# Kernel tuning notes

Hardware: AMD Instinct MI355X
Metric: run time of the kernel (lower is better)

Reference implementation:

```python
import jax, jax.numpy as jnp
import numpy as np

TOPK = 60            # candidates kept by top-k
THRESHOLD = 0.15     # score threshold (post-sigmoid)
NMS_THRESHOLD = 0.05 # IoU overlap for suppression/matching
NMS_TOPK = 20        # max kept detections per image
CROP_SIZE = (96, 96, 96)
AVG_TOPN = 7         # max matched boxes averaged per kept box


def setup_inputs() -> dict:
    key = jax.random.key(0)
    k1, k2, k3 = jax.random.split(key, 3)
    B, D, H, W = 256, 24, 24, 24
    Cls = jax.random.normal(k1, (B, 1, D, H, W), dtype=jnp.float32)
    # sizes in [1,7) voxels so 3D boxes at stride-4 anchor spacing overlap
    Shape = jax.random.uniform(k2, (B, 3, D, H, W), dtype=jnp.float32) * 6.0 + 1.0
    Offset = jax.random.normal(k3, (B, 3, D, H, W), dtype=jnp.float32)
    return {"Cls": Cls, "Shape": Shape, "Offset": Offset}


def _decode(Cls, Shape, Offset):
    # make_anchors + bbox_decode: centers = (anchor + offset) * stride, sizes = Shape
    B, _, D, H, W = Cls.shape
    stride = jnp.float32(CROP_SIZE[0] / D)  # 96/24 = 4
    gz, gy, gx = jnp.meshgrid(jnp.arange(D, dtype=jnp.float32),
                              jnp.arange(H, dtype=jnp.float32),
                              jnp.arange(W, dtype=jnp.float32), indexing="ij")
    anchors = jnp.stack([gz, gy, gx], -1).reshape(-1, 3)            # [N,3]
    scores = jax.nn.sigmoid(Cls.reshape(B, -1))                     # [B,N] (is_logits=True)
    shapes = Shape.reshape(B, 3, -1).transpose(0, 2, 1)             # [B,N,3]
    offsets = Offset.reshape(B, 3, -1).transpose(0, 2, 1)           # [B,N,3]
    centers = (anchors[None] + offsets) * stride
    bboxes = jnp.concatenate([centers, shapes], -1)                 # [B,N,6] = (z,y,x,d,h,w)
    return scores, bboxes


def _iou_matrix(det):
    # axis-aligned 3D IoU between all pairs of the TOPK candidate boxes
    c, s = det[:, 2:5], det[:, 5:8]
    lo, hi = c - 0.5 * s, c + 0.5 * s
    inter = jnp.prod(jnp.maximum(jnp.minimum(hi[:, None], hi[None]) -
                                 jnp.maximum(lo[:, None], lo[None]), 0.0), -1)
    vol = jnp.prod(s, -1)
    return inter / (vol[:, None] + vol[None] - inter)


def _nms_image(scores, bboxes):
    # top-k (sorted descending, as torch.topk) then masked iterative NMS with
    # IoU-matched top-7 box averaging, emitting a fixed [NMS_TOPK, 8] table.
    topk_s, topk_i = jax.lax.top_k(scores, TOPK)
    valid = topk_s > THRESHOLD
    det = jnp.concatenate([jnp.ones((TOPK, 1), jnp.float32),
                           topk_s[:, None], bboxes[topk_i]], -1)    # [TOPK,8]
    iou = _iou_matrix(det)
    ar = jnp.arange(TOPK)

    def step(suppressed, _):
        avail = valid & ~suppressed
        any_avail = jnp.any(avail)
        idx = jnp.argmax(avail)  # first available = highest remaining score
        matched = avail & ((iou[idx] > NMS_THRESHOLD) | (ar == idx))
        rank = jnp.cumsum(matched) - 1            # matched are already score-sorted
        sel = matched & (rank < AVG_TOPN)
        top_n = jnp.minimum(jnp.sum(matched), AVG_TOPN)
        avg = jnp.sum(det * sel[:, None].astype(det.dtype), 0) / jnp.maximum(top_n, 1).astype(det.dtype)
        avg = avg.at[0].set(1.0).at[1].set(det[idx, 1])  # flag=1, prob = best score
        row = jnp.where(top_n > 1, avg, det[idx])
        row = jnp.where(any_avail, row, -jnp.ones(8, det.dtype))
        suppressed = jnp.where(any_avail, suppressed | matched, suppressed)
        return suppressed, row

    _, rows = jax.lax.scan(step, jnp.zeros(TOPK, dtype=bool), None, length=NMS_TOPK)
    return rows  # [NMS_TOPK, 8]


def reference(Cls, Shape, Offset):
    scores, bboxes = _decode(Cls, Shape, Offset)
    return jax.vmap(_nms_image)(scores, bboxes)  # [B, NMS_TOPK, 8]
```

## Files before the change

kernel.cpp:

```cpp
#include <hip/hip_runtime.h>
#include <math.h>

#define N_ANCH 13824
#define TPB 256
#define K_TOP 60
#define K_NMS 20
#define AVG_TOPN 7

__device__ __forceinline__ unsigned mono_key(float x) {
  unsigned m = __float_as_uint(x);
  return (m & 0x80000000u) ? ~m : (m | 0x80000000u);
}

__global__ __launch_bounds__(TPB)
void detpp_kernel(const float* __restrict__ Cls,
                  const float* __restrict__ Shp,
                  const float* __restrict__ Off,
                  float* __restrict__ Out) {
  __shared__ union UMem {
    unsigned int key[N_ANCH];
    float iou[K_TOP][K_TOP];
  } u;
  __shared__ float det[K_TOP][8];
  __shared__ unsigned int hist[256];
  __shared__ unsigned long long cand[64];
  __shared__ unsigned int ccnt;
  __shared__ unsigned int g_prefix;
  __shared__ unsigned int g_r;

  const int b = blockIdx.x;
  const int t = threadIdx.x;
  const int lane = t & 63;

  const float4* C4 = (const float4*)(Cls + (size_t)b * N_ANCH);
  #pragma unroll
  for (int j = 0; j < 13; ++j) {
    int i4 = (j << 8) + t;
    float4 v = C4[i4];
    uint4 k;
    k.x = mono_key(v.x); k.y = mono_key(v.y);
    k.z = mono_key(v.z); k.w = mono_key(v.w);
    ((uint4*)u.key)[i4] = k;
  }
  if (t < 128) {
    int i4 = 3328 + t;
    float4 v = C4[i4];
    uint4 k;
    k.x = mono_key(v.x); k.y = mono_key(v.y);
    k.z = mono_key(v.z); k.w = mono_key(v.w);
    ((uint4*)u.key)[i4] = k;
  }
  if (t == 0) { ccnt = 0; g_prefix = 0; g_r = K_TOP; }
  __syncthreads();

  for (int pass = 0; pass < 4; ++pass) {
    const int shift = 24 - 8 * pass;
    hist[t] = 0;
    __syncthreads();
    const unsigned pref = g_prefix;
    const unsigned rr = g_r;
    for (int j = 0; j < 54; ++j) {
      unsigned k = u.key[(j << 8) | t];
      if (((unsigned long long)(k ^ pref) >> (shift + 8)) == 0ull)
        atomicAdd(&hist[(k >> shift) & 0xffu], 1u);
    }
    __syncthreads();
    if (t < 64) {
      unsigned c0 = hist[4 * lane + 0], c1 = hist[4 * lane + 1];
      unsigned c2 = hist[4 * lane + 2], c3 = hist[4 * lane + 3];
      unsigned pre1 = c0, pre2 = c0 + c1, pre3 = pre2 + c2, pre4 = pre3 + c3;
      unsigned S = pre4;
      #pragma unroll
      for (int d = 1; d < 64; d <<= 1) {
        unsigned o = __shfl_down(S, d, 64);
        if (lane + d < 64) S += o;
      }
      unsigned pre[5] = {0u, pre1, pre2, pre3, pre4};
      int mybin = -1;
      #pragma unroll
      for (int kk = 3; kk >= 0; --kk) {
        if (mybin < 0 && S - pre[kk] >= rr) mybin = kk;
      }
      unsigned long long m = __ballot(mybin >= 0);
      int hl = 63 - __builtin_clzll(m);
      if (lane == hl) {
        g_prefix = pref | ((unsigned)(4 * lane + mybin) << shift);
        g_r = rr - (S - pre[mybin + 1]);
      }
    }
    __syncthreads();
  }

  const unsigned K60 = g_prefix;
  for (int j = 0; j < 54; ++j) {
    int i = (j << 8) | t;
    unsigned k = u.key[i];
    if (k >= K60) {
      unsigned pos = atomicAdd(&ccnt, 1u);
      if (pos < 64) cand[pos] = ((unsigned long long)k << 32) | (unsigned)(~i);
    }
  }
  __syncthreads();

  if (t < 64) {
    unsigned cnt = ccnt; if (cnt > 64u) cnt = 64u;
    unsigned long long klong = (lane < (int)cnt) ? cand[lane] : 0ull;
    unsigned long long v = ~klong;
    #pragma unroll
    for (int k = 2; k <= 64; k <<= 1) {
      #pragma unroll
      for (int j = k >> 1; j > 0; j >>= 1) {
        unsigned long long o = __shfl_xor(v, j, 64);
        bool i_lower = ((lane & j) == 0);
        bool asc = ((lane & k) == 0);
        bool keep_min = (asc == i_lower);
        bool take = keep_min ? (o < v) : (o > v);
        if (take) v = o;
      }
    }
    klong = ~v;
    if (lane < K_TOP) {
      int i = (int)(~(unsigned)(klong & 0xffffffffull));
      unsigned m = (unsigned)(klong >> 32);
      unsigned bits = (m & 0x80000000u) ? (m & 0x7fffffffu) : ~m;
      float lg = __uint_as_float(bits);
      float sc = 1.0f / (1.0f + expf(-lg));
      int iz = i / 576;
      int r2 = i - iz * 576;
      int iy = r2 / 24;
      int ix = r2 - iy * 24;
      size_t bb = (size_t)b * 3 * N_ANCH;
      float o0 = Off[bb + i];
      float o1 = Off[bb + N_ANCH + i];
      float o2 = Off[bb + 2 * N_ANCH + i];
      float s0 = Shp[bb + i];
      float s1 = Shp[bb + N_ANCH + i];
      float s2 = Shp[bb + 2 * N_ANCH + i];
      det[lane][0] = 1.0f;
      det[lane][1] = sc;
      det[lane][2] = ((float)iz + o0) * 4.0f;
      det[lane][3] = ((float)iy + o1) * 4.0f;
      det[lane][4] = ((float)ix + o2) * 4.0f;
      det[lane][5] = s0;
      det[lane][6] = s1;
      det[lane][7] = s2;
    }
  }
  __syncthreads();

  for (int p = t; p < K_TOP * K_TOP; p += TPB) {
    int ii = p / K_TOP;
    int jj = p - ii * K_TOP;
    float cz1 = det[ii][2], cy1 = det[ii][3], cx1 = det[ii][4];
    float sz1 = det[ii][5], sy1 = det[ii][6], sx1 = det[ii][7];
    float cz2 = det[jj][2], cy2 = det[jj][3], cx2 = det[jj][4];
    float sz2 = det[jj][5], sy2 = det[jj][6], sx2 = det[jj][7];
    float lz1 = cz1 - 0.5f * sz1, hz1 = cz1 + 0.5f * sz1;
    float ly1 = cy1 - 0.5f * sy1, hy1 = cy1 + 0.5f * sy1;
    float lx1 = cx1 - 0.5f * sx1, hx1 = cx1 + 0.5f * sx1;
    float lz2 = cz2 - 0.5f * sz2, hz2 = cz2 + 0.5f * sz2;
    float ly2 = cy2 - 0.5f * sy2, hy2 = cy2 + 0.5f * sy2;
    float lx2 = cx2 - 0.5f * sx2, hx2 = cx2 + 0.5f * sx2;
    float dz = fmaxf(fminf(hz1, hz2) - fmaxf(lz1, lz2), 0.0f);
    float dy = fmaxf(fminf(hy1, hy2) - fmaxf(ly1, ly2), 0.0f);
    float dx = fmaxf(fminf(hx1, hx2) - fmaxf(lx1, lx2), 0.0f);
    float inter = (dz * dy) * dx;
    float v1 = (sz1 * sy1) * sx1;
    float v2 = (sz2 * sy2) * sx2;
    u.iou[ii][jj] = inter / (v1 + v2 - inter);
  }
  __syncthreads();

  if (t < 64) {
    const int j = t;
    const bool in = (j < K_TOP);
    float scj = in ? det[j][1] : 0.0f;
    unsigned long long validm = __ballot(in && (scj > 0.15f));
    unsigned long long suppressed = 0ull;
    float* outb = Out + (size_t)b * K_NMS * 8;

    for (int step = 0; step < K_NMS; ++step) {
      unsigned long long avail = validm & ~suppressed;
      if (avail) {
        int idx = __builtin_ctzll(avail);
        bool m = in && ((avail >> j) & 1ull) &&
                 ((u.iou[idx][j] > 0.05f) || (j == idx));
        unsigned long long matched = __ballot(m);
        int cnt = __popcll(matched);
        int top_n = cnt < AVG_TOPN ? cnt : AVG_TOPN;
        if (j < 8) {
          float sum = 0.0f;
          unsigned long long mm = matched;
          for (int q = 0; q < top_n; ++q) {
            int bi = __builtin_ctzll(mm);
            mm &= mm - 1ull;
            sum += det[bi][j];
          }
          float r = sum / (float)top_n;
          if (j == 0) r = 1.0f;
          if (j == 1) r = det[idx][1];
          outb[step * 8 + j] = r;
        }
        suppressed |= matched;
      } else {
        if (j < 8) outb[step * 8 + j] = -1.0f;
      }
    }
  }
}

extern "C" void kernel_launch(void* const* d_in, const int* in_sizes, int n_in,
                              void* d_out, int out_size, void* d_ws, size_t ws_size,
                              hipStream_t stream) {
  const float* Cls = (const float*)d_in[0];
  const float* Shp = (const float*)d_in[1];
  const float* Off = (const float*)d_in[2];
  float* Out = (float*)d_out;
  int B = in_sizes[0] / N_ANCH;
  detpp_kernel<<<B, TPB, 0, stream>>>(Cls, Shp, Off, Out);
}
```

Before: 134.9 us.

## Prefilter top-k candidates with a fixed pivot to shrink radix-select work

The full 13824-key shared-memory array is replaced by a compacted candidate list. Only logits above a fixed pivot (key > 0xC0000000, i.e. logit > 2.0) go into it, and the first-pass histogram is built during the load. Later radix passes and the final gather scan only these few candidates, which also cuts shared-memory use and can raise occupancy. If the candidate count falls outside [60, 1536], it falls back to rescanning Cls from global memory, so correctness holds in general at the cost of extra atomics in the load loop.

Measured after the change: 128.9 us. -4.4%, faster.

```diff
diff --git a/kernel.cpp b/kernel.cpp
--- a/kernel.cpp
+++ b/kernel.cpp
@@ -6,6 +6,8 @@
 #define K_TOP 60
 #define K_NMS 20
 #define AVG_TOPN 7
+#define CAP2 1536
+#define PIVOT_KEY 0xC0000000u
 
 __device__ __forceinline__ unsigned mono_key(float x) {
   unsigned m = __float_as_uint(x);
@@ -18,12 +20,13 @@
                   const float* __restrict__ Off,
                   float* __restrict__ Out) {
   __shared__ union UMem {
-    unsigned int key[N_ANCH];
+    unsigned long long cand2[CAP2];
     float iou[K_TOP][K_TOP];
   } u;
   __shared__ float det[K_TOP][8];
   __shared__ unsigned int hist[256];
   __shared__ unsigned long long cand[64];
+  __shared__ unsigned int cnt2;
   __shared__ unsigned int ccnt;
   __shared__ unsigned int g_prefix;
   __shared__ unsigned int g_r;
@@ -31,40 +34,74 @@
   const int b = blockIdx.x;
   const int t = threadIdx.x;
   const int lane = t & 63;
-
-  const float4* C4 = (const float4*)(Cls + (size_t)b * N_ANCH);
+  const size_t cbase = (size_t)b * N_ANCH;
+
+  if (t == 0) { cnt2 = 0; ccnt = 0; g_prefix = 0u; g_r = K_TOP; }
+  hist[t] = 0;
+  __syncthreads();
+
+  const float4* C4 = (const float4*)(Cls + cbase);
   #pragma unroll
   for (int j = 0; j < 13; ++j) {
     int i4 = (j << 8) + t;
     float4 v = C4[i4];
-    uint4 k;
-    k.x = mono_key(v.x); k.y = mono_key(v.y);
-    k.z = mono_key(v.z); k.w = mono_key(v.w);
-    ((uint4*)u.key)[i4] = k;
+    int i0 = i4 << 2;
+    unsigned kk0 = mono_key(v.x), kk1 = mono_key(v.y);
+    unsigned kk2 = mono_key(v.z), kk3 = mono_key(v.w);
+    unsigned kks[4] = {kk0, kk1, kk2, kk3};
+    #pragma unroll
+    for (int q = 0; q < 4; ++q) {
+      if (kks[q] > PIVOT_KEY) {
+        unsigned pos = atomicAdd(&cnt2, 1u);
+        if (pos < CAP2)
+          u.cand2[pos] = ((unsigned long long)kks[q] << 32) | (unsigned)(~(i0 + q));
+        atomicAdd(&hist[kks[q] >> 24], 1u);
+      }
+    }
   }
   if (t < 128) {
     int i4 = 3328 + t;
     float4 v = C4[i4];
-    uint4 k;
-    k.x = mono_key(v.x); k.y = mono_key(v.y);
-    k.z = mono_key(v.z); k.w = mono_key(v.w);
-    ((uint4*)u.key)[i4] = k;
-  }
-  if (t == 0) { ccnt = 0; g_prefix = 0; g_r = K_TOP; }
-  __syncthreads();
+    int i0 = i4 << 2;
+    unsigned kks[4] = {mono_key(v.x), mono_key(v.y), mono_key(v.z), mono_key(v.w)};
+    #pragma unroll
+    for (int q = 0; q < 4; ++q) {
+      if (kks[q] > PIVOT_KEY) {
+        unsigned pos = atomicAdd(&cnt2, 1u);
+        if (pos < CAP2)
+          u.cand2[pos] = ((unsigned long long)kks[q] << 32) | (unsigned)(~(i0 + q));
+        atomicAdd(&hist[kks[q] >> 24], 1u);
+      }
+    }
+  }
+  __syncthreads();
+
+  const unsigned total = cnt2;
+  const bool fast = (total >= (unsigned)K_TOP) && (total <= (unsigned)CAP2);
 
   for (int pass = 0; pass < 4; ++pass) {
     const int shift = 24 - 8 * pass;
-    hist[t] = 0;
-    __syncthreads();
     const unsigned pref = g_prefix;
     const unsigned rr = g_r;
-    for (int j = 0; j < 54; ++j) {
-      unsigned k = u.key[(j << 8) | t];
-      if (((unsigned long long)(k ^ pref) >> (shift + 8)) == 0ull)
-        atomicAdd(&hist[(k >> shift) & 0xffu], 1u);
-    }
-    __syncthreads();
+    if (pass > 0 || !fast) {
+      hist[t] = 0;
+      __syncthreads();
+      if (fast) {
+        for (unsigned i = t; i < total; i += TPB) {
+          unsigned k = (unsigned)(u.cand2[i] >> 32);
+          if (((k ^ pref) >> (shift + 8)) == 0u)
+            atomicAdd(&hist[(k >> shift) & 0xffu], 1u);
+        }
+      } else {
+        for (int j = 0; j < 54; ++j) {
+          int i = (j << 8) | t;
+          unsigned k = mono_key(Cls[cbase + i]);
+          bool match = (pass == 0) ? true : (((k ^ pref) >> (shift + 8)) == 0u);
+          if (match) atomicAdd(&hist[(k >> shift) & 0xffu], 1u);
+        }
+      }
+      __syncthreads();
+    }
     if (t < 64) {
       unsigned c0 = hist[4 * lane + 0], c1 = hist[4 * lane + 1];
       unsigned c2 = hist[4 * lane + 2], c3 = hist[4 * lane + 3];
@@ -92,12 +129,22 @@
   }
 
   const unsigned K60 = g_prefix;
-  for (int j = 0; j < 54; ++j) {
-    int i = (j << 8) | t;
-    unsigned k = u.key[i];
-    if (k >= K60) {
-      unsigned pos = atomicAdd(&ccnt, 1u);
-      if (pos < 64) cand[pos] = ((unsigned long long)k << 32) | (unsigned)(~i);
+  if (fast) {
+    for (unsigned i = t; i < total; i += TPB) {
+      unsigned long long e = u.cand2[i];
+      if ((unsigned)(e >> 32) >= K60) {
+        unsigned pos = atomicAdd(&ccnt, 1u);
+        if (pos < 64) cand[pos] = e;
+      }
+    }
+  } else {
+    for (int j = 0; j < 54; ++j) {
+      int i = (j << 8) | t;
+      unsigned k = mono_key(Cls[cbase + i]);
+      if (k >= K60) {
+        unsigned pos = atomicAdd(&ccnt, 1u);
+        if (pos < 64) cand[pos] = ((unsigned long long)k << 32) | (unsigned)(~i);
+      }
     }
   }
   __syncthreads();
```

## Prefilter top-k candidates by pivot and use bitmask NMS with parallel decode

Applied to the files above, without the earlier changes.

Loads the class logits into registers and keeps only those above a fixed pivot key in per-thread shared slots. Radix selection then runs over these few candidates instead of all anchors, with a fallback that rescans global memory when the count is too small or slots overflow. The IoU matrix is replaced by per-row match bitmasks built with atomics, box decode is spread over 180 threads, and the NMS averaging is done with wave-level reductions. This cuts shared memory use and per-pass scanning, at the cost of a data-dependent fallback path and extra register pressure.

Measured after the change: 124.8 us. -7.5%, faster.

```diff
diff --git a/kernel.cpp b/kernel.cpp
--- a/kernel.cpp
+++ b/kernel.cpp
@@ -6,6 +6,8 @@
 #define K_TOP 60
 #define K_NMS 20
 #define AVG_TOPN 7
+#define SLOTS 12
+#define PIVOT_KEY 0xC0000000u
 
 __device__ __forceinline__ unsigned mono_key(float x) {
   unsigned m = __float_as_uint(x);
@@ -17,52 +19,84 @@
                   const float* __restrict__ Shp,
                   const float* __restrict__ Off,
                   float* __restrict__ Out) {
-  __shared__ union UMem {
-    unsigned int key[N_ANCH];
-    float iou[K_TOP][K_TOP];
-  } u;
+  __shared__ unsigned long long cand2[TPB * SLOTS];
   __shared__ float det[K_TOP][8];
+  __shared__ unsigned long long Mrow[K_TOP];
   __shared__ unsigned int hist[256];
   __shared__ unsigned long long cand[64];
-  __shared__ unsigned int ccnt;
-  __shared__ unsigned int g_prefix;
-  __shared__ unsigned int g_r;
+  __shared__ unsigned long long selk[64];
+  __shared__ unsigned int ccnt, totcnt, oflow;
+  __shared__ unsigned int g_prefix, g_r;
 
   const int b = blockIdx.x;
   const int t = threadIdx.x;
   const int lane = t & 63;
-
-  const float4* C4 = (const float4*)(Cls + (size_t)b * N_ANCH);
-  #pragma unroll
-  for (int j = 0; j < 13; ++j) {
-    int i4 = (j << 8) + t;
-    float4 v = C4[i4];
-    uint4 k;
-    k.x = mono_key(v.x); k.y = mono_key(v.y);
-    k.z = mono_key(v.z); k.w = mono_key(v.w);
-    ((uint4*)u.key)[i4] = k;
-  }
-  if (t < 128) {
-    int i4 = 3328 + t;
-    float4 v = C4[i4];
-    uint4 k;
-    k.x = mono_key(v.x); k.y = mono_key(v.y);
-    k.z = mono_key(v.z); k.w = mono_key(v.w);
-    ((uint4*)u.key)[i4] = k;
-  }
-  if (t == 0) { ccnt = 0; g_prefix = 0; g_r = K_TOP; }
-  __syncthreads();
-
+  const size_t cbase = (size_t)b * N_ANCH;
+
+  if (t == 0) { ccnt = 0; totcnt = 0; oflow = 0; g_prefix = 0u; g_r = K_TOP; }
+  if (t < K_TOP) Mrow[t] = 0ull;
+
+  const float4* C4 = (const float4*)(Cls + cbase);
+  float4 v[14];
+  #pragma unroll
+  for (int j = 0; j < 13; ++j) v[j] = C4[(j << 8) + t];
+  if (t < 128) v[13] = C4[3328 + t];
+
+  int cnt = 0;
+  const int base = t * SLOTS;
+  auto process = [&](float4 val, int i0) {
+    float a[4] = {val.x, val.y, val.z, val.w};
+    #pragma unroll
+    for (int q = 0; q < 4; ++q) {
+      unsigned k = mono_key(a[q]);
+      if (k > PIVOT_KEY) {
+        if (cnt < SLOTS)
+          cand2[base + cnt] = ((unsigned long long)k << 32) | (unsigned)(~(i0 + q));
+        cnt++;
+      }
+    }
+  };
+  #pragma unroll
+  for (int j = 0; j < 13; ++j) process(v[j], ((j << 8) + t) << 2);
+  if (t < 128) process(v[13], (3328 + t) << 2);
+
+  int wsum = cnt;
+  #pragma unroll
+  for (int d = 1; d < 64; d <<= 1) wsum += __shfl_xor(wsum, d, 64);
+  unsigned long long ofm = __ballot(cnt > SLOTS);
+  if (lane == 0) {
+    atomicAdd(&totcnt, (unsigned)wsum);
+    if (ofm) atomicOr(&oflow, 1u);
+  }
+  __syncthreads();
+  const unsigned total = totcnt;
+  const bool fast = (total >= (unsigned)K_TOP) && (oflow == 0u);
+  const int myn = cnt < SLOTS ? cnt : SLOTS;
+
+  #pragma unroll
   for (int pass = 0; pass < 4; ++pass) {
     const int shift = 24 - 8 * pass;
     hist[t] = 0;
     __syncthreads();
     const unsigned pref = g_prefix;
     const unsigned rr = g_r;
-    for (int j = 0; j < 54; ++j) {
-      unsigned k = u.key[(j << 8) | t];
-      if (((unsigned long long)(k ^ pref) >> (shift + 8)) == 0ull)
-        atomicAdd(&hist[(k >> shift) & 0xffu], 1u);
+    if (fast) {
+      for (int kk = 0; kk < myn; ++kk) {
+        unsigned k = (unsigned)(cand2[base + kk] >> 32);
+        bool match;
+        if (pass == 0) match = true;
+        else match = (((k ^ pref) >> (shift + 8)) == 0u);
+        if (match) atomicAdd(&hist[(k >> shift) & 0xffu], 1u);
+      }
+    } else {
+      for (int j = 0; j < 54; ++j) {
+        int i = (j << 8) | t;
+        unsigned k = mono_key(Cls[cbase + i]);
+        bool match;
+        if (pass == 0) match = true;
+        else match = (((k ^ pref) >> (shift + 8)) == 0u);
+        if (match) atomicAdd(&hist[(k >> shift) & 0xffu], 1u);
+      }
     }
     __syncthreads();
     if (t < 64) {
@@ -92,59 +126,69 @@
   }
 
   const unsigned K60 = g_prefix;
-  for (int j = 0; j < 54; ++j) {
-    int i = (j << 8) | t;
-    unsigned k = u.key[i];
-    if (k >= K60) {
-      unsigned pos = atomicAdd(&ccnt, 1u);
-      if (pos < 64) cand[pos] = ((unsigned long long)k << 32) | (unsigned)(~i);
+  if (fast) {
+    for (int kk = 0; kk < myn; ++kk) {
+      unsigned long long e = cand2[base + kk];
+      if ((unsigned)(e >> 32) >= K60) {
+        unsigned pos = atomicAdd(&ccnt, 1u);
+        if (pos < 64) cand[pos] = e;
+      }
+    }
+  } else {
+    for (int j = 0; j < 54; ++j) {
+      int i = (j << 8) | t;
+      unsigned k = mono_key(Cls[cbase + i]);
+      if (k >= K60) {
+        unsigned pos = atomicAdd(&ccnt, 1u);
+        if (pos < 64) cand[pos] = ((unsigned long long)k << 32) | (unsigned)(~i);
+      }
     }
   }
   __syncthreads();
 
   if (t < 64) {
-    unsigned cnt = ccnt; if (cnt > 64u) cnt = 64u;
-    unsigned long long klong = (lane < (int)cnt) ? cand[lane] : 0ull;
-    unsigned long long v = ~klong;
+    unsigned cc = ccnt; if (cc > 64u) cc = 64u;
+    unsigned long long klong = (lane < (int)cc) ? cand[lane] : 0ull;
+    unsigned long long vv = ~klong;
     #pragma unroll
     for (int k = 2; k <= 64; k <<= 1) {
       #pragma unroll
       for (int j = k >> 1; j > 0; j >>= 1) {
-        unsigned long long o = __shfl_xor(v, j, 64);
+        unsigned long long o = __shfl_xor(vv, j, 64);
         bool i_lower = ((lane & j) == 0);
         bool asc = ((lane & k) == 0);
         bool keep_min = (asc == i_lower);
-        bool take = keep_min ? (o < v) : (o > v);
-        if (take) v = o;
-      }
-    }
-    klong = ~v;
-    if (lane < K_TOP) {
-      int i = (int)(~(unsigned)(klong & 0xffffffffull));
-      unsigned m = (unsigned)(klong >> 32);
-      unsigned bits = (m & 0x80000000u) ? (m & 0x7fffffffu) : ~m;
-      float lg = __uint_as_float(bits);
-      float sc = 1.0f / (1.0f + expf(-lg));
-      int iz = i / 576;
-      int r2 = i - iz * 576;
-      int iy = r2 / 24;
-      int ix = r2 - iy * 24;
-      size_t bb = (size_t)b * 3 * N_ANCH;
-      float o0 = Off[bb + i];
-      float o1 = Off[bb + N_ANCH + i];
-      float o2 = Off[bb + 2 * N_ANCH + i];
-      float s0 = Shp[bb + i];
-      float s1 = Shp[bb + N_ANCH + i];
-      float s2 = Shp[bb + 2 * N_ANCH + i];
-      det[lane][0] = 1.0f;
-      det[lane][1] = sc;
-      det[lane][2] = ((float)iz + o0) * 4.0f;
-      det[lane][3] = ((float)iy + o1) * 4.0f;
-      det[lane][4] = ((float)ix + o2) * 4.0f;
-      det[lane][5] = s0;
-      det[lane][6] = s1;
-      det[lane][7] = s2;
-    }
+        bool take = keep_min ? (o < vv) : (o > vv);
+        if (take) vv = o;
+      }
+    }
+    selk[lane] = ~vv;
+  }
+  __syncthreads();
+
+  if (t < 180) {
+    int e = t / 3;
+    int f = t - 3 * e;
+    unsigned long long kl = selk[e];
+    int i = (int)(~(unsigned)(kl & 0xffffffffull));
+    int iz = i / 576;
+    int r2 = i - iz * 576;
+    int iy = r2 / 24;
+    int ix = r2 - iy * 24;
+    int a = (f == 0) ? iz : ((f == 1) ? iy : ix);
+    size_t bb = (size_t)b * 3 * N_ANCH + (size_t)f * N_ANCH + (size_t)i;
+    float o = Off[bb];
+    float s = Shp[bb];
+    det[e][2 + f] = ((float)a + o) * 4.0f;
+    det[e][5 + f] = s;
+  } else if (t < 240) {
+    int e = t - 180;
+    unsigned long long kl = selk[e];
+    unsigned m = (unsigned)(kl >> 32);
+    unsigned bits = (m & 0x80000000u) ? (m & 0x7fffffffu) : ~m;
+    float lg = __uint_as_float(bits);
+    det[e][0] = 1.0f;
+    det[e][1] = 1.0f / (1.0f + expf(-lg));
   }
   __syncthreads();
 
@@ -167,44 +211,52 @@
     float inter = (dz * dy) * dx;
     float v1 = (sz1 * sy1) * sx1;
     float v2 = (sz2 * sy2) * sx2;
-    u.iou[ii][jj] = inter / (v1 + v2 - inter);
+    float iouv = inter / (v1 + v2 - inter);
+    if ((iouv > 0.05f) || (jj == ii)) atomicOr(&Mrow[ii], 1ull << jj);
   }
   __syncthreads();
 
   if (t < 64) {
-    const int j = t;
-    const bool in = (j < K_TOP);
-    float scj = in ? det[j][1] : 0.0f;
-    unsigned long long validm = __ballot(in && (scj > 0.15f));
+    const bool in = (lane < K_TOP);
+    float myscore = in ? det[lane][1] : 0.0f;
+    unsigned long long M = in ? Mrow[lane] : 0ull;
+    unsigned long long validm = __ballot(in && (myscore > 0.15f));
     unsigned long long suppressed = 0ull;
     float* outb = Out + (size_t)b * K_NMS * 8;
-
+    const int q = lane >> 3, c = lane & 7;
+
+    #pragma unroll
     for (int step = 0; step < K_NMS; ++step) {
       unsigned long long avail = validm & ~suppressed;
-      if (avail) {
-        int idx = __builtin_ctzll(avail);
-        bool m = in && ((avail >> j) & 1ull) &&
-                 ((u.iou[idx][j] > 0.05f) || (j == idx));
-        unsigned long long matched = __ballot(m);
-        int cnt = __popcll(matched);
-        int top_n = cnt < AVG_TOPN ? cnt : AVG_TOPN;
-        if (j < 8) {
-          float sum = 0.0f;
-          unsigned long long mm = matched;
-          for (int q = 0; q < top_n; ++q) {
-            int bi = __builtin_ctzll(mm);
-            mm &= mm - 1ull;
-            sum += det[bi][j];
-          }
-          float r = sum / (float)top_n;
-          if (j == 0) r = 1.0f;
-          if (j == 1) r = det[idx][1];
-          outb[step * 8 + j] = r;
-        }
-        suppressed |= matched;
-      } else {
-        if (j < 8) outb[step * 8 + j] = -1.0f;
-      }
+      const bool any = (avail != 0ull);
+      int idx = any ? (int)__builtin_ctzll(avail) : 0;
+      unsigned mlo = (unsigned)__builtin_amdgcn_readlane((int)(unsigned)(M & 0xffffffffull), idx);
+      unsigned mhi = (unsigned)__builtin_amdgcn_readlane((int)(unsigned)(M >> 32), idx);
+      unsigned long long matched = any ? (avail & (((unsigned long long)mhi << 32) | mlo)) : 0ull;
+      int cm = __popcll(matched);
+      int top_n = cm < AVG_TOPN ? cm : AVG_TOPN;
+      int myb = 0;
+      { unsigned long long m2 = matched;
+        #pragma unroll
+        for (int z = 0; z < 8; ++z) {
+          int bz = m2 ? (int)__builtin_ctzll(m2) : 0;
+          if (z == q) myb = bz;
+          m2 &= m2 - 1ull;
+        } }
+      float vv = (q < top_n) ? det[myb][c] : 0.0f;
+      vv += __shfl_xor(vv, 8, 64);
+      vv += __shfl_xor(vv, 16, 64);
+      vv += __shfl_xor(vv, 32, 64);
+      float sidx = __uint_as_float((unsigned)__builtin_amdgcn_readlane((int)__float_as_uint(myscore), idx));
+      float r = vv / (float)(top_n > 0 ? top_n : 1);
+      if (lane < 8) {
+        float o = r;
+        if (lane == 0) o = 1.0f;
+        if (lane == 1) o = sidx;
+        if (!any) o = -1.0f;
+        outb[step * 8 + lane] = o;
+      }
+      suppressed |= matched;
     }
   }
 }
```
